# Kernel tuning notes

Measured on AMD Instinct MI355X. Metric: run time of the kernel, lower is better.

Reference implementation:

```python
import jax, jax.numpy as jnp
import numpy as np

B, N, C = 2, 1024, 512
H = 8
HD = C // H  # 64
SCALE = HD ** -0.5


def setup_inputs() -> dict:
    key = jax.random.key(0)
    ks = jax.random.split(key, 10)
    q = jax.random.normal(ks[0], (B, N, C), jnp.float32)
    k = jax.random.normal(ks[1], (B, N, C), jnp.float32)
    v = jax.random.normal(ks[2], (B, N, C), jnp.float32)
    rel_pos_bias = jax.random.normal(ks[3], (B, N, N, HD), jnp.float32)
    # float padding mask: 0 for valid tokens, large negative for padded ones
    key_padding_mask = jnp.where(
        jax.random.uniform(ks[4], (B, N)) > 0.1, 0.0, -1e4
    ).astype(jnp.float32)
    Wq = jax.random.normal(ks[5], (C, C), jnp.float32) * 0.02
    Wk = jax.random.normal(ks[6], (C, C), jnp.float32) * 0.02
    Wv = jax.random.normal(ks[7], (C, C), jnp.float32) * 0.02
    Wp = jax.random.normal(ks[8], (C, C), jnp.float32) * 0.02
    bp = jnp.zeros((C,), jnp.float32)
    return {"q": q, "k": k, "v": v, "rel_pos_bias": rel_pos_bias,
            "key_padding_mask": key_padding_mask,
            "Wq": Wq, "Wk": Wk, "Wv": Wv, "Wp": Wp, "bp": bp}


def reference(q, k, v, rel_pos_bias, key_padding_mask, Wq, Wk, Wv, Wp, bp):
    # QKV projections, split heads: [B,H,N,HD]
    qh = (q @ Wq).reshape(B, N, H, HD).transpose(0, 2, 1, 3) * SCALE
    kh = (k @ Wk).reshape(B, N, H, HD).transpose(0, 2, 1, 3)
    vh = (v @ Wv).reshape(B, N, H, HD).transpose(0, 2, 1, 3)
    # scores + relative-bias injection into logits
    attn = jnp.einsum('bhid,bhjd->bhij', qh, kh)
    attn = attn + jnp.einsum('bhic,bijc->bhij', qh, rel_pos_bias)
    # float padding mask -> pairwise additive bias
    m = key_padding_mask
    pair = jnp.minimum(m[:, None, :], m[:, :, None])
    pair = jnp.where(jnp.maximum(m[:, None, :], m[:, :, None]) < 0, 0.0, pair)
    attn = attn + pair[:, None, :, :]
    attn = jax.nn.softmax(attn, axis=-1)
    # weighted values, with relative-bias injection into output
    x = jnp.einsum('bhij,bhjd->bihd', attn, vh)
    x = x + jnp.einsum('bhij,bijc->bihc', attn, rel_pos_bias)
    x = x.reshape(B, N, H * HD)
    return x @ Wp + bp
```

## Files before the change

kernel.cpp:

```cpp
#include <hip/hip_runtime.h>
#include <hip/hip_bf16.h>


typedef __attribute__((ext_vector_type(8))) short short8;
typedef __attribute__((ext_vector_type(4))) short short4v;
typedef __attribute__((ext_vector_type(4))) float f32x4;

#if defined(__has_builtin)
#  if __has_builtin(__builtin_amdgcn_mfma_f32_16x16x16bf16_1k)
#    define HAVE_MFMA16 1
#  endif
#endif
#ifndef HAVE_MFMA16
#  define HAVE_MFMA16 0
#endif

__device__ __forceinline__ unsigned short f2b(float f) {
    union { float f; unsigned u; } v; v.f = f;
    unsigned r = (v.u + 0x7FFF + ((v.u >> 16) & 1)) >> 16;
    return (unsigned short)r;
}
__device__ __forceinline__ float b2f(unsigned short h) {
    union { unsigned u; float f; } v; v.u = ((unsigned)h) << 16;
    return v.f;
}

__device__ __forceinline__ unsigned cvt_pk(float a, float b) {
    unsigned r;
    asm("v_cvt_pk_bf16_f32 %0, %1, %2" : "=v"(r) : "v"(a), "v"(b));
    return r;
}

#define LGKM0_BAR()                                            \
    do {                                                       \
        asm volatile("s_waitcnt lgkmcnt(0)" ::: "memory");     \
        __builtin_amdgcn_s_barrier();                          \
        asm volatile("" ::: "memory");                         \
    } while (0)

__global__ __launch_bounds__(256) void wprep(
    const float* __restrict__ W0, const float* __restrict__ W1,
    const float* __restrict__ W2, const float* __restrict__ W3,
    unsigned short* __restrict__ WT)
{
    const int z = blockIdx.z;
    const float* W = (z == 0) ? W0 : ((z == 1) ? W1 : ((z == 2) ? W2 : W3));
    __shared__ float Ts[64][65];
    const int t = threadIdx.x;
    const int k0 = blockIdx.x * 64, n0 = blockIdx.y * 64;
    const int kr = t >> 2, nc = (t & 3) * 16;
    #pragma unroll
    for (int q = 0; q < 4; ++q) {
        float4 v = *reinterpret_cast<const float4*>(
            W + (size_t)(k0 + kr) * 512 + n0 + nc + q * 4);
        Ts[kr][nc + q * 4 + 0] = v.x; Ts[kr][nc + q * 4 + 1] = v.y;
        Ts[kr][nc + q * 4 + 2] = v.z; Ts[kr][nc + q * 4 + 3] = v.w;
    }
    __syncthreads();
    const int nl = t >> 2, kc = (t & 3) * 16;
    if (z < 3) {
        unsigned short* T = WT + (size_t)z * 262144;
        unsigned short tmp[16];
        #pragma unroll
        for (int e = 0; e < 16; ++e) tmp[e] = f2b(Ts[kc + e][nl]);
        unsigned short* dst = T + (size_t)(n0 + nl) * 512 + k0 + kc;
        *reinterpret_cast<short8*>(dst)     = *reinterpret_cast<short8*>(&tmp[0]);
        *reinterpret_cast<short8*>(dst + 8) = *reinterpret_cast<short8*>(&tmp[8]);
    } else {
        unsigned short* Th = WT + (size_t)3 * 262144;
        unsigned short* Tl = WT + (size_t)4 * 262144;
        unsigned short hi[16], lo[16];
        #pragma unroll
        for (int e = 0; e < 16; ++e) {
            float v = Ts[kc + e][nl];
            hi[e] = f2b(v);
            lo[e] = f2b(v - b2f(hi[e]));
        }
        unsigned short* dh = Th + (size_t)(n0 + nl) * 512 + k0 + kc;
        unsigned short* dl = Tl + (size_t)(n0 + nl) * 512 + k0 + kc;
        *reinterpret_cast<short8*>(dh)     = *reinterpret_cast<short8*>(&hi[0]);
        *reinterpret_cast<short8*>(dh + 8) = *reinterpret_cast<short8*>(&hi[8]);
        *reinterpret_cast<short8*>(dl)     = *reinterpret_cast<short8*>(&lo[0]);
        *reinterpret_cast<short8*>(dl + 8) = *reinterpret_cast<short8*>(&lo[8]);
    }
}

__global__ __launch_bounds__(256) void proj_mfma(
    const float* __restrict__ qg, const float* __restrict__ kg,
    const float* __restrict__ vg, const unsigned short* __restrict__ WT,
    unsigned short* __restrict__ qhb, unsigned short* __restrict__ khb,
    unsigned short* __restrict__ vtb)
{
    const int z = blockIdx.z;
    const float* X = (z == 0) ? qg : ((z == 1) ? kg : vg);
    const unsigned short* WTz = WT + (size_t)z * 262144;
    const float scale = (z == 0) ? 0.125f : 1.0f;

    __shared__ unsigned short As[64][72];
    const int t = threadIdx.x, w = t >> 6, l = t & 63;
    const int l16 = l & 15, lg = l >> 4;
    const int m0 = blockIdx.x * 64, n0 = blockIdx.y * 64;
    const int ra = t >> 2, kc = (t & 3) * 16;

    f32x4 acc[4];
    #pragma unroll
    for (int cs = 0; cs < 4; ++cs) acc[cs] = 0.0f;

    for (int k0 = 0; k0 < 512; k0 += 64) {
        float4 va[4];
        #pragma unroll
        for (int qq = 0; qq < 4; ++qq)
            va[qq] = *reinterpret_cast<const float4*>(
                X + (size_t)(m0 + ra) * 512 + k0 + kc + qq * 4);
        uint4 pk0, pk1;
        pk0.x = cvt_pk(va[0].x, va[0].y); pk0.y = cvt_pk(va[0].z, va[0].w);
        pk0.z = cvt_pk(va[1].x, va[1].y); pk0.w = cvt_pk(va[1].z, va[1].w);
        pk1.x = cvt_pk(va[2].x, va[2].y); pk1.y = cvt_pk(va[2].z, va[2].w);
        pk1.z = cvt_pk(va[3].x, va[3].y); pk1.w = cvt_pk(va[3].z, va[3].w);
        __syncthreads();
        *reinterpret_cast<uint4*>(&As[ra][kc])     = pk0;
        *reinterpret_cast<uint4*>(&As[ra][kc + 8]) = pk1;
        __syncthreads();
        #pragma unroll
        for (int kk = 0; kk < 2; ++kk) {
            short8 a = *reinterpret_cast<const short8*>(
                &As[w * 16 + l16][kk * 32 + 8 * lg]);
            #pragma unroll
            for (int cs = 0; cs < 4; ++cs) {
                short8 b = *reinterpret_cast<const short8*>(
                    WTz + (size_t)(n0 + cs * 16 + l16) * 512 + k0 + kk * 32 + 8 * lg);
                acc[cs] = __builtin_amdgcn_mfma_f32_16x16x32_bf16(a, b, acc[cs], 0, 0, 0);
            }
        }
    }

    const int h = blockIdx.y;
    if (z < 2) {
        unsigned short* Y = (z == 0) ? qhb : khb;
        #pragma unroll
        for (int cs = 0; cs < 4; ++cs)
            #pragma unroll
            for (int r = 0; r < 4; ++r) {
                int m = m0 + w * 16 + lg * 4 + r;
                int bb = m >> 10, nn = m & 1023;
                Y[(((size_t)((bb * 8 + h) * 1024 + nn)) << 6) + cs * 16 + l16] =
                    f2b(acc[cs][r] * scale);
            }
    } else {
        int mbase = m0 + w * 16 + lg * 4;
        int bb = mbase >> 10, nn = mbase & 1023;
        #pragma unroll
        for (int cs = 0; cs < 4; ++cs) {
            ushort4 o;
            o.x = f2b(acc[cs][0]); o.y = f2b(acc[cs][1]);
            o.z = f2b(acc[cs][2]); o.w = f2b(acc[cs][3]);
            *reinterpret_cast<ushort4*>(
                vtb + (((size_t)(bb * 8 + h) * 64 + cs * 16 + l16) << 10) + nn) = o;
        }
    }
}

__global__ __launch_bounds__(256) void out_mfma(
    const float* __restrict__ xpart, const float* __restrict__ lsump,
    const unsigned short* __restrict__ WT, const float* __restrict__ bp,
    float* __restrict__ out)
{
    const unsigned short* WPhi = WT + (size_t)3 * 262144;
    const unsigned short* WPlo = WT + (size_t)4 * 262144;
    __shared__ unsigned short Ah[64][72];
    __shared__ unsigned short Al[64][72];
    const int t = threadIdx.x, w = t >> 6, l = t & 63;
    const int l16 = l & 15, lg = l >> 4;
    const int m0 = blockIdx.x * 64, n0 = blockIdx.y * 64;
    const int ra = t >> 2, kc = (t & 3) * 16;
    const int mrow = m0 + ra, bb = mrow >> 10, nn = mrow & 1023;

    f32x4 acc[4];
    #pragma unroll
    for (int cs = 0; cs < 4; ++cs) acc[cs] = 0.0f;

    for (int k0 = 0; k0 < 512; k0 += 64) {
        const int h = k0 >> 6;
        float ls = lsump[(bb * 8 + h) * 1024 + nn]
                 + lsump[16384 + (bb * 8 + h) * 1024 + nn];
        float inv = 1.0f / ls;
        unsigned short hi[16], lo[16];
        #pragma unroll
        for (int qq = 0; qq < 4; ++qq) {
            size_t base = ((size_t)(bb * 1024 + nn)) * 512 + k0 + kc + qq * 4;
            float4 v0 = *reinterpret_cast<const float4*>(xpart + base);
            float4 v1 = *reinterpret_cast<const float4*>(xpart + (1u << 20) + base);
            float e0 = (v0.x + v1.x) * inv, e1 = (v0.y + v1.y) * inv;
            float e2 = (v0.z + v1.z) * inv, e3 = (v0.w + v1.w) * inv;
            hi[qq * 4 + 0] = f2b(e0); lo[qq * 4 + 0] = f2b(e0 - b2f(hi[qq * 4 + 0]));
            hi[qq * 4 + 1] = f2b(e1); lo[qq * 4 + 1] = f2b(e1 - b2f(hi[qq * 4 + 1]));
            hi[qq * 4 + 2] = f2b(e2); lo[qq * 4 + 2] = f2b(e2 - b2f(hi[qq * 4 + 2]));
            hi[qq * 4 + 3] = f2b(e3); lo[qq * 4 + 3] = f2b(e3 - b2f(hi[qq * 4 + 3]));
        }
        __syncthreads();
        *reinterpret_cast<short8*>(&Ah[ra][kc])     = *reinterpret_cast<short8*>(&hi[0]);
        *reinterpret_cast<short8*>(&Ah[ra][kc + 8]) = *reinterpret_cast<short8*>(&hi[8]);
        *reinterpret_cast<short8*>(&Al[ra][kc])     = *reinterpret_cast<short8*>(&lo[0]);
        *reinterpret_cast<short8*>(&Al[ra][kc + 8]) = *reinterpret_cast<short8*>(&lo[8]);
        __syncthreads();
        #pragma unroll
        for (int kk = 0; kk < 2; ++kk) {
            short8 ah = *reinterpret_cast<const short8*>(
                &Ah[w * 16 + l16][kk * 32 + 8 * lg]);
            short8 al = *reinterpret_cast<const short8*>(
                &Al[w * 16 + l16][kk * 32 + 8 * lg]);
            #pragma unroll
            for (int cs = 0; cs < 4; ++cs) {
                size_t wb = (size_t)(n0 + cs * 16 + l16) * 512 + k0 + kk * 32 + 8 * lg;
                short8 bh = *reinterpret_cast<const short8*>(WPhi + wb);
                short8 bl = *reinterpret_cast<const short8*>(WPlo + wb);
                acc[cs] = __builtin_amdgcn_mfma_f32_16x16x32_bf16(ah, bh, acc[cs], 0, 0, 0);
                acc[cs] = __builtin_amdgcn_mfma_f32_16x16x32_bf16(ah, bl, acc[cs], 0, 0, 0);
                acc[cs] = __builtin_amdgcn_mfma_f32_16x16x32_bf16(al, bh, acc[cs], 0, 0, 0);
            }
        }
    }

    #pragma unroll
    for (int cs = 0; cs < 4; ++cs) {
        int col = n0 + cs * 16 + l16;
        float bv = bp[col];
        #pragma unroll
        for (int r = 0; r < 4; ++r) {
            int row = m0 + w * 16 + lg * 4 + r;
            out[(size_t)row * 512 + col] = acc[cs][r] + bv;
        }
    }
}

__global__ __launch_bounds__(512, 2) void attn_mfma(
    const unsigned short* __restrict__ qhg, const unsigned short* __restrict__ khg,
    const unsigned short* __restrict__ vtg, const float* __restrict__ rpb,
    const float* __restrict__ mask, float* __restrict__ xpart,
    float* __restrict__ lsump)
{
    __shared__ unsigned short rpb_s[2][16][16][72];
    __shared__ unsigned short khs[8][16][72];
    __shared__ unsigned short vts[8][64][24];
    __shared__ unsigned short q1[8][16][72];
    __shared__ unsigned short P[8][16][40];
    __shared__ float S2s[16][8][17];
    __shared__ float mask_s[512];

    const int bid = blockIdx.x;
    const int js = bid & 1, it = (bid >> 1) & 63, b = bid >> 7;
    const int i0 = it * 16, jb = js * 512;
    const int t = threadIdx.x, w = t >> 6, l = t & 63;
    const int lg = l >> 4, l16 = l & 15;

    const int sj = (t >> 3) & 15, sc = (t & 7) * 8, sib = t >> 7;
    const int kh_h = t >> 6, kh_j = (t >> 2) & 15, kh_c = (t & 3) * 16;
    const int vt_h = t >> 6, vt_c = t & 63;

    const float* rpbb = rpb + ((size_t)(b * 1024 + i0) << 16);

#define RPB_ISSUE(PF, J0)                                                      \
    _Pragma("unroll")                                                          \
    for (int itr = 0; itr < 4; ++itr) {                                        \
        const float4* s_ = reinterpret_cast<const float4*>(                    \
            rpbb + ((size_t)(sib + 4 * itr) << 16) +                           \
            (size_t)((J0) + sj) * 64 + sc);                                    \
        PF[2 * itr] = s_[0]; PF[2 * itr + 1] = s_[1];                          \
    }

#define RPB_WRITE(PF, BUF)                                                     \
    _Pragma("unroll")                                                          \
    for (int itr = 0; itr < 4; ++itr) {                                        \
        float4 ua = PF[2 * itr], ub = PF[2 * itr + 1];                         \
        uint4 pk;                                                              \
        pk.x = cvt_pk(ua.x, ua.y); pk.y = cvt_pk(ua.z, ua.w);                  \
        pk.z = cvt_pk(ub.x, ub.y); pk.w = cvt_pk(ub.z, ub.w);                  \
        *reinterpret_cast<uint4*>(&rpb_s[BUF][sib + 4 * itr][sj][sc]) = pk;    \
    }

#define KH_ISSUE(KP, J0)                                                       \
    {                                                                          \
        const unsigned short* p_ = khg + ((size_t)(b * 8 + kh_h) << 16) +      \
            (size_t)((J0) + kh_j) * 64 + kh_c;                                 \
        KP[0] = *reinterpret_cast<const short8*>(p_);                          \
        KP[1] = *reinterpret_cast<const short8*>(p_ + 8);                      \
    }

#define KH_WRITE(KP)                                                           \
    {                                                                          \
        *reinterpret_cast<short8*>(&khs[kh_h][kh_j][kh_c])     = KP[0];        \
        *reinterpret_cast<short8*>(&khs[kh_h][kh_j][kh_c + 8]) = KP[1];        \
    }

#define VT_ISSUE(VP, J0)                                                       \
    {                                                                          \
        const unsigned short* p_ = vtg + ((size_t)(b * 8 + vt_h) << 16) +      \
            ((size_t)vt_c << 10) + (J0);                                       \
        VP[0] = *reinterpret_cast<const short8*>(p_);                          \
        VP[1] = *reinterpret_cast<const short8*>(p_ + 8);                      \
    }

#define VT_WRITE(VP)                                                           \
    {                                                                          \
        *reinterpret_cast<short8*>(&vts[vt_h][vt_c][0]) = VP[0];               \
        *reinterpret_cast<short8*>(&vts[vt_h][vt_c][8]) = VP[1];               \
    }

    {
        int h = t >> 6, i = (t >> 2) & 15, c = (t & 3) * 16;
        const short8* src = reinterpret_cast<const short8*>(
            qhg + (((size_t)(b * 8 + h) * 1024 + i0 + i) << 6) + c);
        *reinterpret_cast<short8*>(&q1[h][i][c])     = src[0];
        *reinterpret_cast<short8*>(&q1[h][i][c + 8]) = src[1];
    }
    if (t < 128) {
        *reinterpret_cast<float4*>(&mask_s[t * 4]) =
            *reinterpret_cast<const float4*>(&mask[b * 1024 + jb + t * 4]);
    }
    {
        unsigned short* P1 = &P[0][0][0];
        #pragma unroll
        for (int r = 0; r < 10; ++r) P1[t + 512 * r] = 0;
    }
    float mrow[4];
    #pragma unroll
    for (int r = 0; r < 4; r++) mrow[r] = mask[b * 1024 + i0 + lg * 4 + r];

    float4 pfA[8], pfB[8];
    short8 kpfA[2], kpfB[2], vpfA[2], vpfB[2];
    RPB_ISSUE(pfA, jb)
    KH_ISSUE(kpfA, jb)
    VT_ISSUE(vpfA, jb)

    LGKM0_BAR();

    short8 a1[2];
    a1[0] = *reinterpret_cast<const short8*>(&q1[w][l16][8 * lg]);
    a1[1] = *reinterpret_cast<const short8*>(&q1[w][l16][32 + 8 * lg]);
    short8 bq[2][2];
    #pragma unroll
    for (int il = 0; il < 2; ++il) {
        bq[il][0] = *reinterpret_cast<const short8*>(
            &q1[l16 & 7][2 * w + il][8 * lg]);
        bq[il][1] = *reinterpret_cast<const short8*>(
            &q1[l16 & 7][2 * w + il][32 + 8 * lg]);
    }

    const int jo = (lg < 2) ? 8 * lg : 0;
    const int ro = jo;
    (void)ro;

    f32x4 x1[4];
    #pragma unroll
    for (int cs = 0; cs < 4; cs++) x1[cs] = 0.0f;
    f32x4 x2[2][4];
    #pragma unroll
    for (int il = 0; il < 2; il++)
        #pragma unroll
        for (int cg = 0; cg < 4; cg++) x2[il][cg] = 0.0f;
    float lsum[4] = {0.f, 0.f, 0.f, 0.f};

#define ATTN_ITER(T, PFC, KPC, VPC, PFN, KPN, VPN)                             \
    {                                                                          \
        const int jt = (T);                                                    \
        const int cur = jt & 1;                                                \
        const int j0 = jb + jt * 16;                                           \
        if (jt < 31) {                                                         \
            RPB_ISSUE(PFN, j0 + 16)                                            \
            KH_ISSUE(KPN, j0 + 16)                                             \
            VT_ISSUE(VPN, j0 + 16)                                             \
        }                                                                      \
        RPB_WRITE(PFC, cur)                                                    \
        KH_WRITE(KPC)                                                          \
        VT_WRITE(VPC)                                                          \
        LGKM0_BAR();                                                           \
        f32x4 C1; C1 = 0.0f;                                                   \
        {                                                                      \
            short8 kb0 = *reinterpret_cast<const short8*>(&khs[w][l16][8 * lg]); \
            short8 kb1 = *reinterpret_cast<const short8*>(&khs[w][l16][32 + 8 * lg]); \
            C1 = __builtin_amdgcn_mfma_f32_16x16x32_bf16(a1[0], kb0, C1, 0, 0, 0); \
            C1 = __builtin_amdgcn_mfma_f32_16x16x32_bf16(a1[1], kb1, C1, 0, 0, 0); \
        }                                                                      \
        _Pragma("unroll")                                                      \
        for (int il = 0; il < 2; ++il) {                                       \
            int i = 2 * w + il;                                                \
            f32x4 D2; D2 = 0.0f;                                               \
            _Pragma("unroll")                                                  \
            for (int ch = 0; ch < 2; ++ch) {                                   \
                short8 ar = *reinterpret_cast<const short8*>(                  \
                    &rpb_s[cur][i][l16][ch * 32 + 8 * lg]);                    \
                D2 = __builtin_amdgcn_mfma_f32_16x16x32_bf16(ar, bq[il][ch], D2, 0, 0, 0); \
            }                                                                  \
            if (l16 < 8) {                                                     \
                _Pragma("unroll")                                              \
                for (int r = 0; r < 4; ++r)                                    \
                    S2s[i][l16][4 * lg + r] = D2[r];                           \
            }                                                                  \
        }                                                                      \
        LGKM0_BAR();                                                           \
        {                                                                      \
            float mj = mask_s[jt * 16 + l16];                                  \
            _Pragma("unroll")                                                  \
            for (int r = 0; r < 4; ++r) {                                      \
                int ir = lg * 4 + r;                                           \
                float mi = mrow[r];                                            \
                float pm = (fmaxf(mi, mj) < 0.f) ? 0.f : fminf(mi, mj);        \
                float s = C1[r] + S2s[ir][w][l16] + pm;                        \
                float p = __expf(s);                                           \
                lsum[r] += p;                                                  \
                P[w][ir][l16] = f2b(p);                                        \
            }                                                                  \
        }                                                                      \
        LGKM0_BAR();                                                           \
        X1X2_BODY(cur)                                                         \
        LGKM0_BAR();                                                           \
    }

#if HAVE_MFMA16
#define X1X2_BODY(CUR)                                                         \
    {                                                                          \
        short4v pa = *reinterpret_cast<const short4v*>(&P[w][l16][4 * lg]);    \
        _Pragma("unroll")                                                      \
        for (int cs = 0; cs < 4; ++cs) {                                       \
            short4v vb = *reinterpret_cast<const short4v*>(                    \
                &vts[w][cs * 16 + l16][4 * lg]);                               \
            x1[cs] = __builtin_amdgcn_mfma_f32_16x16x16bf16_1k(pa, vb, x1[cs], 0, 0, 0); \
        }                                                                      \
    }                                                                          \
    _Pragma("unroll")                                                          \
    for (int il = 0; il < 2; ++il) {                                           \
        int i = 2 * w + il;                                                    \
        short4v pa2 = *reinterpret_cast<const short4v*>(&P[l16 & 7][i][4 * lg]); \
        _Pragma("unroll")                                                      \
        for (int cg = 0; cg < 4; ++cg) {                                       \
            short4v bb;                                                        \
            _Pragma("unroll")                                                  \
            for (int e = 0; e < 4; ++e)                                        \
                bb[e] = (short)rpb_s[CUR][i][4 * lg + e][cg * 16 + l16];       \
            x2[il][cg] = __builtin_amdgcn_mfma_f32_16x16x16bf16_1k(pa2, bb, x2[il][cg], 0, 0, 0); \
        }                                                                      \
    }
#else
#define X1X2_BODY(CUR)                                                         \
    {                                                                          \
        short8 pa = *reinterpret_cast<const short8*>(&P[w][l16][8 * lg]);      \
        _Pragma("unroll")                                                      \
        for (int cs = 0; cs < 4; ++cs) {                                       \
            short8 vb = *reinterpret_cast<const short8*>(                      \
                &vts[w][cs * 16 + l16][jo]);                                   \
            x1[cs] = __builtin_amdgcn_mfma_f32_16x16x32_bf16(pa, vb, x1[cs], 0, 0, 0); \
        }                                                                      \
    }                                                                          \
    _Pragma("unroll")                                                          \
    for (int il = 0; il < 2; ++il) {                                           \
        int i = 2 * w + il;                                                    \
        short8 pa2 = *reinterpret_cast<const short8*>(&P[l16 & 7][i][8 * lg]); \
        _Pragma("unroll")                                                      \
        for (int cg = 0; cg < 4; ++cg) {                                       \
            short8 bb;                                                         \
            _Pragma("unroll")                                                  \
            for (int e = 0; e < 8; ++e)                                        \
                bb[e] = (short)rpb_s[CUR][i][ro + e][cg * 16 + l16];           \
            x2[il][cg] = __builtin_amdgcn_mfma_f32_16x16x32_bf16(pa2, bb, x2[il][cg], 0, 0, 0); \
        }                                                                      \
    }
#endif

    for (int th = 0; th < 16; ++th) {
        ATTN_ITER(2 * th,     pfA, kpfA, vpfA, pfB, kpfB, vpfB)
        ATTN_ITER(2 * th + 1, pfB, kpfB, vpfB, pfA, kpfA, vpfA)
    }

    #pragma unroll
    for (int r = 0; r < 4; ++r) {
        float v = lsum[r];
        v += __shfl_xor(v, 1, 64); v += __shfl_xor(v, 2, 64);
        v += __shfl_xor(v, 4, 64); v += __shfl_xor(v, 8, 64);
        lsum[r] = v;
    }

    __syncthreads();
    float* x2s = reinterpret_cast<float*>(&rpb_s[0][0][0][0]);
    if (lg < 2) {
        #pragma unroll
        for (int il = 0; il < 2; ++il)
            #pragma unroll
            for (int cg = 0; cg < 4; ++cg)
                #pragma unroll
                for (int r = 0; r < 4; ++r)
                    x2s[((2 * w + il) * 8 + 4 * lg + r) * 64 + cg * 16 + l16] =
                        x2[il][cg][r];
    }
    __syncthreads();

    #pragma unroll
    for (int cs = 0; cs < 4; ++cs)
        #pragma unroll
        for (int r = 0; r < 4; ++r) {
            int ir = lg * 4 + r;
            float val = x1[cs][r] + x2s[(ir * 8 + w) * 64 + cs * 16 + l16];
            xpart[((size_t)js << 20) + ((size_t)(b * 1024 + i0 + ir)) * 512
                  + w * 64 + cs * 16 + l16] = val;
        }
    if (l16 == 0) {
        #pragma unroll
        for (int r = 0; r < 4; ++r)
            lsump[((size_t)js << 14) + (b * 8 + w) * 1024 + i0 + lg * 4 + r] = lsum[r];
    }
#undef ATTN_ITER
#undef X1X2_BODY
#undef RPB_ISSUE
#undef RPB_WRITE
#undef KH_ISSUE
#undef KH_WRITE
#undef VT_ISSUE
#undef VT_WRITE
}

extern "C" void kernel_launch(void* const* d_in, const int* in_sizes, int n_in,
                              void* d_out, int out_size, void* d_ws, size_t ws_size,
                              hipStream_t stream)
{
    (void)in_sizes; (void)n_in; (void)out_size; (void)ws_size;
    const float* q    = (const float*)d_in[0];
    const float* k    = (const float*)d_in[1];
    const float* v    = (const float*)d_in[2];
    const float* rpb  = (const float*)d_in[3];
    const float* mask = (const float*)d_in[4];
    const float* Wq   = (const float*)d_in[5];
    const float* Wk   = (const float*)d_in[6];
    const float* Wv   = (const float*)d_in[7];
    const float* Wp   = (const float*)d_in[8];
    const float* bp   = (const float*)d_in[9];
    float* out = (float*)d_out;

    unsigned short* qhb = (unsigned short*)d_ws;
    unsigned short* khb = qhb + 1048576;
    unsigned short* vtb = khb + 1048576;
    float* xpart = (float*)(vtb + 1048576);
    float* lsump = xpart + 2097152;
    unsigned short* wT = (unsigned short*)(lsump + 32768);

    wprep<<<dim3(8, 8, 4), 256, 0, stream>>>(Wq, Wk, Wv, Wp, wT);

    proj_mfma<<<dim3(32, 8, 3), 256, 0, stream>>>(q, k, v, wT, qhb, khb, vtb);

    attn_mfma<<<256, 512, 0, stream>>>(qhb, khb, vtb, rpb, mask, xpart, lsump);

    out_mfma<<<dim3(32, 8), 256, 0, stream>>>(xpart, lsump, wT, bp, out);
}
```

Measured before the change: 185.1 us.

## Double-buffer K/V tiles in LDS, swizzle K layout, and drop per-iteration barriers

```diff
diff --git a/kernel.cpp b/kernel.cpp
--- a/kernel.cpp
+++ b/kernel.cpp
@@ -240,13 +240,11 @@
     float* __restrict__ lsump)
 {
     __shared__ unsigned short rpb_s[2][16][16][72];
-    __shared__ unsigned short khs[8][16][72];
-    __shared__ unsigned short vts[8][64][24];
-    __shared__ unsigned short q1[8][16][72];
+    __shared__ unsigned short khs2[2][8][16][64];
+    __shared__ unsigned short vts2[2][8][64][16];
     __shared__ unsigned short P[8][16][40];
     __shared__ float S2s[16][8][17];
     __shared__ float mask_s[512];
-
     const int bid = blockIdx.x;
     const int js = bid & 1, it = (bid >> 1) & 63, b = bid >> 7;
     const int i0 = it * 16, jb = js * 512;
@@ -286,10 +284,11 @@
         KP[1] = *reinterpret_cast<const short8*>(p_ + 8);                      \
     }
 
-#define KH_WRITE(KP)                                                           \
-    {                                                                          \
-        *reinterpret_cast<short8*>(&khs[kh_h][kh_j][kh_c])     = KP[0];        \
-        *reinterpret_cast<short8*>(&khs[kh_h][kh_j][kh_c + 8]) = KP[1];        \
+#define KH_WRITE(KP, BUF)                                                      \
+    {                                                                          \
+        int s_ = kh_j & 7, c0_ = kh_c >> 3;                                    \
+        *reinterpret_cast<short8*>(&khs2[BUF][kh_h][kh_j][(c0_ ^ s_) * 8]) = KP[0]; \
+        *reinterpret_cast<short8*>(&khs2[BUF][kh_h][kh_j][((c0_ + 1) ^ s_) * 8]) = KP[1]; \
     }
 
 #define VT_ISSUE(VP, J0)                                                       \
@@ -300,12 +299,14 @@
         VP[1] = *reinterpret_cast<const short8*>(p_ + 8);                      \
     }
 
-#define VT_WRITE(VP)                                                           \
-    {                                                                          \
-        *reinterpret_cast<short8*>(&vts[vt_h][vt_c][0]) = VP[0];               \
-        *reinterpret_cast<short8*>(&vts[vt_h][vt_c][8]) = VP[1];               \
-    }
-
+#define VT_WRITE(VP, BUF)                                                      \
+    {                                                                          \
+        *reinterpret_cast<short8*>(&vts2[BUF][vt_h][vt_c][0]) = VP[0];         \
+        *reinterpret_cast<short8*>(&vts2[BUF][vt_h][vt_c][8]) = VP[1];         \
+    }
+
+    unsigned short (*q1)[16][72] =
+        reinterpret_cast<unsigned short (*)[16][72]>(&khs2[0][0][0][0]);
     {
         int h = t >> 6, i = (t >> 2) & 15, c = (t & 3) * 16;
         const short8* src = reinterpret_cast<const short8*>(
@@ -346,6 +347,8 @@
             &q1[l16 & 7][2 * w + il][32 + 8 * lg]);
     }
 
+    LGKM0_BAR();
+
     const int jo = (lg < 2) ? 8 * lg : 0;
     const int ro = jo;
     (void)ro;
@@ -359,6 +362,58 @@
         #pragma unroll
         for (int cg = 0; cg < 4; cg++) x2[il][cg] = 0.0f;
     float lsum[4] = {0.f, 0.f, 0.f, 0.f};
+
+#if HAVE_MFMA16
+#define X1_BODY(CUR)                                                           \
+    {                                                                          \
+        short4v pa = *reinterpret_cast<const short4v*>(&P[w][l16][4 * lg]);    \
+        _Pragma("unroll")                                                      \
+        for (int cs = 0; cs < 4; ++cs) {                                       \
+            short4v vb = *reinterpret_cast<const short4v*>(                    \
+                &vts2[CUR][w][cs * 16 + l16][4 * lg]);                         \
+            x1[cs] = __builtin_amdgcn_mfma_f32_16x16x16bf16_1k(pa, vb, x1[cs], 0, 0, 0); \
+        }                                                                      \
+    }
+#define X2_BODY(CUR)                                                           \
+    _Pragma("unroll")                                                          \
+    for (int il = 0; il < 2; ++il) {                                           \
+        int i = 2 * w + il;                                                    \
+        short4v pa2 = *reinterpret_cast<const short4v*>(&P[l16 & 7][i][4 * lg]); \
+        _Pragma("unroll")                                                      \
+        for (int cg = 0; cg < 4; ++cg) {                                       \
+            short4v bb;                                                        \
+            _Pragma("unroll")                                                  \
+            for (int e = 0; e < 4; ++e)                                        \
+                bb[e] = (short)rpb_s[CUR][i][4 * lg + e][cg * 16 + l16];       \
+            x2[il][cg] = __builtin_amdgcn_mfma_f32_16x16x16bf16_1k(pa2, bb, x2[il][cg], 0, 0, 0); \
+        }                                                                      \
+    }
+#else
+#define X1_BODY(CUR)                                                           \
+    {                                                                          \
+        short8 pa = *reinterpret_cast<const short8*>(&P[w][l16][8 * lg]);      \
+        _Pragma("unroll")                                                      \
+        for (int cs = 0; cs < 4; ++cs) {                                       \
+            short8 vb = *reinterpret_cast<const short8*>(                      \
+                &vts2[CUR][w][cs * 16 + l16][jo]);                             \
+            x1[cs] = __builtin_amdgcn_mfma_f32_16x16x32_bf16(pa, vb, x1[cs], 0, 0, 0); \
+        }                                                                      \
+    }
+#define X2_BODY(CUR)                                                           \
+    _Pragma("unroll")                                                          \
+    for (int il = 0; il < 2; ++il) {                                           \
+        int i = 2 * w + il;                                                    \
+        short8 pa2 = *reinterpret_cast<const short8*>(&P[l16 & 7][i][8 * lg]); \
+        _Pragma("unroll")                                                      \
+        for (int cg = 0; cg < 4; ++cg) {                                       \
+            short8 bb;                                                         \
+            _Pragma("unroll")                                                  \
+            for (int e = 0; e < 8; ++e)                                        \
+                bb[e] = (short)rpb_s[CUR][i][ro + e][cg * 16 + l16];           \
+            x2[il][cg] = __builtin_amdgcn_mfma_f32_16x16x32_bf16(pa2, bb, x2[il][cg], 0, 0, 0); \
+        }                                                                      \
+    }
+#endif
 
 #define ATTN_ITER(T, PFC, KPC, VPC, PFN, KPN, VPN)                             \
     {                                                                          \
@@ -371,13 +426,15 @@
             VT_ISSUE(VPN, j0 + 16)                                             \
         }                                                                      \
         RPB_WRITE(PFC, cur)                                                    \
-        KH_WRITE(KPC)                                                          \
-        VT_WRITE(VPC)                                                          \
-        LGKM0_BAR();                                                           \
+        KH_WRITE(KPC, cur)                                                     \
+        VT_WRITE(VPC, cur)                                                     \
+        LGKM0_BAR();                           \
         f32x4 C1; C1 = 0.0f;                                                   \
         {                                                                      \
-            short8 kb0 = *reinterpret_cast<const short8*>(&khs[w][l16][8 * lg]); \
-            short8 kb1 = *reinterpret_cast<const short8*>(&khs[w][l16][32 + 8 * lg]); \
+            short8 kb0 = *reinterpret_cast<const short8*>(                     \
+                &khs2[cur][w][l16][(lg ^ (l16 & 7)) * 8]);                     \
+            short8 kb1 = *reinterpret_cast<const short8*>(                     \
+                &khs2[cur][w][l16][((4 + lg) ^ (l16 & 7)) * 8]);               \
             C1 = __builtin_amdgcn_mfma_f32_16x16x32_bf16(a1[0], kb0, C1, 0, 0, 0); \
             C1 = __builtin_amdgcn_mfma_f32_16x16x32_bf16(a1[1], kb1, C1, 0, 0, 0); \
         }                                                                      \
@@ -397,7 +454,7 @@
                     S2s[i][l16][4 * lg + r] = D2[r];                           \
             }                                                                  \
         }                                                                      \
-        LGKM0_BAR();                                                           \
+        LGKM0_BAR();                                      \
         {                                                                      \
             float mj = mask_s[jt * 16 + l16];                                  \
             _Pragma("unroll")                                                  \
@@ -411,60 +468,11 @@
                 P[w][ir][l16] = f2b(p);                                        \
             }                                                                  \
         }                                                                      \
-        LGKM0_BAR();                                                           \
-        X1X2_BODY(cur)                                                         \
-        LGKM0_BAR();                                                           \
-    }
-
-#if HAVE_MFMA16
-#define X1X2_BODY(CUR)                                                         \
-    {                                                                          \
-        short4v pa = *reinterpret_cast<const short4v*>(&P[w][l16][4 * lg]);    \
-        _Pragma("unroll")                                                      \
-        for (int cs = 0; cs < 4; ++cs) {                                       \
-            short4v vb = *reinterpret_cast<const short4v*>(                    \
-                &vts[w][cs * 16 + l16][4 * lg]);                               \
-            x1[cs] = __builtin_amdgcn_mfma_f32_16x16x16bf16_1k(pa, vb, x1[cs], 0, 0, 0); \
-        }                                                                      \
-    }                                                                          \
-    _Pragma("unroll")                                                          \
-    for (int il = 0; il < 2; ++il) {                                           \
-        int i = 2 * w + il;                                                    \
-        short4v pa2 = *reinterpret_cast<const short4v*>(&P[l16 & 7][i][4 * lg]); \
-        _Pragma("unroll")                                                      \
-        for (int cg = 0; cg < 4; ++cg) {                                       \
-            short4v bb;                                                        \
-            _Pragma("unroll")                                                  \
-            for (int e = 0; e < 4; ++e)                                        \
-                bb[e] = (short)rpb_s[CUR][i][4 * lg + e][cg * 16 + l16];       \
-            x2[il][cg] = __builtin_amdgcn_mfma_f32_16x16x16bf16_1k(pa2, bb, x2[il][cg], 0, 0, 0); \
-        }                                                                      \
-    }
-#else
-#define X1X2_BODY(CUR)                                                         \
-    {                                                                          \
-        short8 pa = *reinterpret_cast<const short8*>(&P[w][l16][8 * lg]);      \
-        _Pragma("unroll")                                                      \
-        for (int cs = 0; cs < 4; ++cs) {                                       \
-            short8 vb = *reinterpret_cast<const short8*>(                      \
-                &vts[w][cs * 16 + l16][jo]);                                   \
-            x1[cs] = __builtin_amdgcn_mfma_f32_16x16x32_bf16(pa, vb, x1[cs], 0, 0, 0); \
-        }                                                                      \
-    }                                                                          \
-    _Pragma("unroll")                                                          \
-    for (int il = 0; il < 2; ++il) {                                           \
-        int i = 2 * w + il;                                                    \
-        short8 pa2 = *reinterpret_cast<const short8*>(&P[l16 & 7][i][8 * lg]); \
-        _Pragma("unroll")                                                      \
-        for (int cg = 0; cg < 4; ++cg) {                                       \
-            short8 bb;                                                         \
-            _Pragma("unroll")                                                  \
-            for (int e = 0; e < 8; ++e)                                        \
-                bb[e] = (short)rpb_s[CUR][i][ro + e][cg * 16 + l16];           \
-            x2[il][cg] = __builtin_amdgcn_mfma_f32_16x16x32_bf16(pa2, bb, x2[il][cg], 0, 0, 0); \
-        }                                                                      \
-    }
-#endif
+        X1_BODY(cur)            \
+        LGKM0_BAR();                      \
+        X2_BODY(cur)                                                           \
+         \
+    }
 
     for (int th = 0; th < 16; ++th) {
         ATTN_ITER(2 * th,     pfA, kpfA, vpfA, pfB, kpfB, vpfB)
@@ -508,7 +516,8 @@
             lsump[((size_t)js << 14) + (b * 8 + w) * 1024 + i0 + lg * 4 + r] = lsum[r];
     }
 #undef ATTN_ITER
-#undef X1X2_BODY
+#undef X1_BODY
+#undef X2_BODY
 #undef RPB_ISSUE
 #undef RPB_WRITE
 #undef KH_ISSUE
```

Measured after the change: 188.1 us. No clear change (+1.6%).
